# Performance work log

Measured on AMD Instinct MI355X. Metric: run time of the kernel, lower is better.

The kernel has to match this reference:

```python
import jax, jax.numpy as jnp
import numpy as np
import math

MODEL_DIM = 1024
NUM_HEADS = 16
ATTN_DIM = MODEL_DIM // NUM_HEADS  # 64
ROWS, COLS, AXES = 32, 32, 2
PAIRS = ATTN_DIM // (AXES * 2)     # 16
BATCH = 4
TOKENS = ROWS * COLS               # 1024


def setup_inputs() -> dict:
    key = jax.random.key(0)
    ks = jax.random.split(key, 8)
    s = 1.0 / math.sqrt(MODEL_DIM)
    return {
        "x": jax.random.normal(ks[0], (BATCH, TOKENS, MODEL_DIM), jnp.float32),
        "cos": jax.random.uniform(ks[1], (ROWS, COLS, AXES, PAIRS), jnp.float32),
        "sin": jax.random.uniform(ks[2], (ROWS, COLS, AXES, PAIRS), jnp.float32),
        "Wq": jax.random.normal(ks[3], (MODEL_DIM, MODEL_DIM), jnp.float32) * s,
        "Wk": jax.random.normal(ks[4], (MODEL_DIM, MODEL_DIM), jnp.float32) * s,
        "Wv": jax.random.normal(ks[5], (MODEL_DIM, MODEL_DIM), jnp.float32) * s,
        "Wo": jax.random.normal(ks[6], (MODEL_DIM, MODEL_DIM), jnp.float32) * s,
        "bo": jax.random.normal(ks[7], (MODEL_DIM,), jnp.float32) * 0.01,
    }


def _apply_rope(W, cos, sin):
    # W: (b, h, tokens, attn_dim) -> (b, h, rows, cols, axes, pairs, 2)
    b, h, n, d = W.shape
    rows, cols, axes, pairs = cos.shape
    Wp = W.reshape(b, h, rows, cols, axes, pairs, 2)
    c = cos[None, None]
    s = sin[None, None]
    w0, w1 = Wp[..., 0], Wp[..., 1]
    out = jnp.stack([c * w0 - s * w1, s * w0 + c * w1], axis=-1)
    return out.reshape(b, h, n, d)


def reference(x, cos, sin, Wq, Wk, Wv, Wo, bo):
    b, n, _ = x.shape
    # torch Linear: y = x @ W.T
    Q = (x @ Wq.T).reshape(b, n, NUM_HEADS, ATTN_DIM).transpose(0, 2, 1, 3)
    K = (x @ Wk.T).reshape(b, n, NUM_HEADS, ATTN_DIM).transpose(0, 2, 1, 3)
    V = (x @ Wv.T).reshape(b, n, NUM_HEADS, ATTN_DIM).transpose(0, 2, 1, 3)
    Q = _apply_rope(Q, cos, sin)
    K = _apply_rope(K, cos, sin)
    scores = jnp.einsum("bhqd,bhkd->bhqk", Q, K) / math.sqrt(ATTN_DIM)
    attn = jax.nn.softmax(scores, axis=-1)
    o = jnp.einsum("bhqk,bhkd->bhqd", attn, V)
    o = o.transpose(0, 2, 1, 3).reshape(b, n, MODEL_DIM)
    return o @ Wo.T + bo
```

## Files before the change

### kernel.cpp

```cpp
#include <hip/hip_runtime.h>
#include <hip/hip_bf16.h>

typedef __bf16 bf16;
typedef __bf16 bf16x4 __attribute__((ext_vector_type(4)));
typedef __bf16 bf16x8 __attribute__((ext_vector_type(8)));
typedef float  f32x4  __attribute__((ext_vector_type(4)));
typedef unsigned int u32x2 __attribute__((ext_vector_type(2)));

#define MFMA16(a, b, c) __builtin_amdgcn_mfma_f32_16x16x32_bf16((a), (b), (c), 0, 0, 0)

#define GLOBAL_AS(p) ((const __attribute__((address_space(1))) void*)(p))
#define LDS_AS(p)    ((__attribute__((address_space(3))) void*)(p))

#define BATCH 4
#define TOK   1024
#define DIM   1024
#define HEADS 16
#define HD    64
#define MTOT  (BATCH * TOK)
#define MELEM (1024u * 1024u)

__global__ __launch_bounds__(256) void k_prep(
    const float* __restrict__ X,
    const float* __restrict__ W0, const float* __restrict__ W1,
    const float* __restrict__ W2, const float* __restrict__ W3,
    bf16* __restrict__ xh, bf16* __restrict__ wsp)
{
    const int bid = blockIdx.x;
    if (bid < 2048) {
        size_t i0 = ((size_t)bid * 256 + threadIdx.x) * 8;
        f32x4 a = *(const f32x4*)(X + i0);
        f32x4 b = *(const f32x4*)(X + i0 + 4);
        bf16x8 h;
        #pragma unroll
        for (int j = 0; j < 4; j++) { h[j] = (bf16)a[j]; h[4 + j] = (bf16)b[j]; }
        *(bf16x8*)(xh + i0) = h;
    } else {
        const int b2 = bid - 2048;
        const int widx = b2 >> 9;
        const int inner = b2 & 511;
        const float* W = (widx == 0) ? W0 : (widx == 1) ? W1 : (widx == 2) ? W2 : W3;
        size_t i0 = ((size_t)inner * 256 + threadIdx.x) * 8;
        f32x4 a = *(const f32x4*)(W + i0);
        f32x4 b = *(const f32x4*)(W + i0 + 4);
        bf16x8 h, l;
        #pragma unroll
        for (int j = 0; j < 4; j++) {
            bf16 g0 = (bf16)a[j]; h[j] = g0;     l[j] = (bf16)(a[j] - (float)g0);
            bf16 g1 = (bf16)b[j]; h[4 + j] = g1; l[4 + j] = (bf16)(b[j] - (float)g1);
        }
        *(bf16x8*)(wsp + (size_t)widx * MELEM + i0) = h;
        if (widx == 3)
            *(bf16x8*)(wsp + 4 * (size_t)MELEM + i0) = l;
    }
}

__global__ __launch_bounds__(512) void k_gemmQKV(
    const bf16* __restrict__ Ag, const bf16* __restrict__ wsp,
    const float* __restrict__ cosT, const float* __restrict__ sinT,
    bf16* __restrict__ q_o, bf16* __restrict__ k_o, bf16* __restrict__ v_o)
{
    __shared__ bf16 Alin[128 * 64];
    __shared__ bf16 Blin[256 * 64];

    const int fid = blockIdx.x;
    const int swz = (fid & 7) * 48 + (fid >> 3);
    const int nt = swz % 12;
    const int mt = swz / 12;

    const int t = threadIdx.x;
    const int lane = t & 63;
    const int w = t >> 6;
    const int wr = w >> 2, wc = w & 3;
    const int l15 = lane & 15;

    f32x4 acc[4][4];
    #pragma unroll
    for (int m = 0; m < 4; m++)
        #pragma unroll
        for (int n = 0; n < 4; n++)
            #pragma unroll
            for (int r = 0; r < 4; r++) acc[m][n][r] = 0.f;

    const int srow = lane >> 3;
    const int schk8 = ((lane & 7) ^ (srow & 7)) * 8;
    const bf16* asrc = Ag  + (size_t)(mt * 128 + srow) * DIM + schk8;
    const bf16* bsrc = wsp + (size_t)(nt * 256 + srow) * DIM + schk8;

    for (int k0 = 0; k0 < DIM; k0 += 64) {
        __syncthreads();
        #pragma unroll
        for (int ii = 0; ii < 2; ++ii) {
            int i = w * 2 + ii;
            __builtin_amdgcn_global_load_lds(
                GLOBAL_AS(asrc + (size_t)i * 8 * DIM + k0),
                LDS_AS(&Alin[i * 512]), 16, 0, 0);
        }
        #pragma unroll
        for (int jj = 0; jj < 4; ++jj) {
            int j = w * 4 + jj;
            __builtin_amdgcn_global_load_lds(
                GLOBAL_AS(bsrc + (size_t)j * 8 * DIM + k0),
                LDS_AS(&Blin[j * 512]), 16, 0, 0);
        }
        __syncthreads();

        #pragma unroll
        for (int ks = 0; ks < 2; ks++) {
            const int cc = (lane >> 4) + ks * 4;
            bf16x8 fb[4];
            #pragma unroll
            for (int n = 0; n < 4; n++) {
                int rb = wc * 64 + n * 16 + l15;
                fb[n] = *(const bf16x8*)&Blin[rb * 64 + ((cc ^ (rb & 7)) << 3)];
            }
            #pragma unroll
            for (int m = 0; m < 4; m++) {
                int r = wr * 64 + m * 16 + l15;
                bf16x8 fa = *(const bf16x8*)&Alin[r * 64 + ((cc ^ (r & 7)) << 3)];
                #pragma unroll
                for (int n = 0; n < 4; n++)
                    acc[m][n] = MFMA16(fa, fb[n], acc[m][n]);
            }
        }
    }

    const int mode = nt >> 2;
    const int h = (nt & 3) * 4 + wc;
    if (mode == 2) {
        #pragma unroll
        for (int m = 0; m < 4; m++) {
            const int grow0 = mt * 128 + wr * 64 + m * 16 + (lane >> 4) * 4;
            const int b = grow0 >> 10, ntok0 = grow0 & (TOK - 1);
            #pragma unroll
            for (int n = 0; n < 4; n++) {
                const int d = n * 16 + l15;
                bf16x4 pk;
                #pragma unroll
                for (int r = 0; r < 4; r++) pk[r] = (bf16)acc[m][n][r];
                *(bf16x4*)&v_o[((size_t)((b * HEADS + h) * HD + d)) * TOK + ntok0] = pk;
            }
        }
    } else {
        __syncthreads();
        float* cosL = (float*)Alin;
        float* sinL = (float*)Blin;
        const int tb = (mt & 7) * 128;
        *(f32x4*)(cosL + t * 8)     = *(const f32x4*)(cosT + (size_t)tb * 32 + t * 8);
        *(f32x4*)(cosL + t * 8 + 4) = *(const f32x4*)(cosT + (size_t)tb * 32 + t * 8 + 4);
        *(f32x4*)(sinL + t * 8)     = *(const f32x4*)(sinT + (size_t)tb * 32 + t * 8);
        *(f32x4*)(sinL + t * 8 + 4) = *(const f32x4*)(sinT + (size_t)tb * 32 + t * 8 + 4);
        __syncthreads();

        bf16* dst = (mode == 0) ? q_o : k_o;
        const float sc = (mode == 0) ? 0.18033688f : 1.0f;
        #pragma unroll
        for (int m = 0; m < 4; m++) {
            const int grow0 = mt * 128 + wr * 64 + m * 16 + (lane >> 4) * 4;
            const int b = grow0 >> 10, ntok0 = grow0 & (TOK - 1);
            const int loc0 = wr * 64 + m * 16 + (lane >> 4) * 4;
            #pragma unroll
            for (int n = 0; n < 4; n++) {
                const int d = n * 16 + l15;
                const int idp = (d >> 5) * 16 + ((d >> 1) & 15);
                const bool ev = (d & 1) == 0;
                #pragma unroll
                for (int r = 0; r < 4; r++) {
                    float v = acc[m][n][r];
                    float pr = __shfl_xor(v, 1, 64);
                    float c = cosL[(loc0 + r) * 32 + idp];
                    float s = sinL[(loc0 + r) * 32 + idp];
                    float res = (ev ? (c * v - s * pr) : (s * pr + c * v)) * sc;
                    dst[((size_t)(b * HEADS + h) * TOK + ntok0 + r) * HD + d] = (bf16)res;
                }
            }
        }
    }
}

__global__ __launch_bounds__(256) void k_gemmO(
    const bf16* __restrict__ Ag, const bf16* __restrict__ wsp,
    const float* __restrict__ bo, float* __restrict__ f_o)
{
    __shared__ bf16 Alin[64 * 64];
    __shared__ bf16 Bhlin[128 * 64];
    __shared__ bf16 Bllin[128 * 64];

    const bf16* Bh_g = wsp + 3 * (size_t)MELEM;
    const bf16* Bl_g = wsp + 4 * (size_t)MELEM;

    const int fid = blockIdx.x;
    const int swz = (fid & 7) * 64 + (fid >> 3);
    const int nt = swz & 7;
    const int mt = swz >> 3;

    const int t = threadIdx.x;
    const int lane = t & 63;
    const int w = t >> 6;
    const int wr = w >> 1, wc = w & 1;
    const int l15 = lane & 15;

    f32x4 acc[2][4];
    #pragma unroll
    for (int m = 0; m < 2; m++)
        #pragma unroll
        for (int n = 0; n < 4; n++)
            #pragma unroll
            for (int r = 0; r < 4; r++) acc[m][n][r] = 0.f;

    const int srow = lane >> 3;
    const int schk8 = ((lane & 7) ^ (srow & 7)) * 8;
    const bf16* asrc  = Ag   + (size_t)(mt * 64 + srow) * DIM + schk8;
    const bf16* bhsrc = Bh_g + (size_t)(nt * 128 + srow) * DIM + schk8;
    const bf16* blsrc = Bl_g + (size_t)(nt * 128 + srow) * DIM + schk8;

    for (int k0 = 0; k0 < DIM; k0 += 64) {
        __syncthreads();
        #pragma unroll
        for (int ii = 0; ii < 2; ++ii) {
            int i = w * 2 + ii;
            __builtin_amdgcn_global_load_lds(
                GLOBAL_AS(asrc + (size_t)i * 8 * DIM + k0),
                LDS_AS(&Alin[i * 512]), 16, 0, 0);
        }
        #pragma unroll
        for (int jj = 0; jj < 4; ++jj) {
            int j = w * 4 + jj;
            size_t roff = (size_t)j * 8 * DIM + k0;
            __builtin_amdgcn_global_load_lds(GLOBAL_AS(bhsrc + roff),
                                             LDS_AS(&Bhlin[j * 512]), 16, 0, 0);
            __builtin_amdgcn_global_load_lds(GLOBAL_AS(blsrc + roff),
                                             LDS_AS(&Bllin[j * 512]), 16, 0, 0);
        }
        __syncthreads();

        #pragma unroll
        for (int ks = 0; ks < 2; ks++) {
            const int cc = (lane >> 4) + ks * 4;
            bf16x8 fbh[4], fbl[4];
            #pragma unroll
            for (int n = 0; n < 4; n++) {
                int r = wc * 64 + n * 16 + l15;
                int off = r * 64 + ((cc ^ (r & 7)) << 3);
                fbh[n] = *(const bf16x8*)&Bhlin[off];
                fbl[n] = *(const bf16x8*)&Bllin[off];
            }
            #pragma unroll
            for (int m = 0; m < 2; m++) {
                int r = wr * 32 + m * 16 + l15;
                bf16x8 fa = *(const bf16x8*)&Alin[r * 64 + ((cc ^ (r & 7)) << 3)];
                #pragma unroll
                for (int n = 0; n < 4; n++) {
                    acc[m][n] = MFMA16(fa, fbh[n], acc[m][n]);
                    acc[m][n] = MFMA16(fa, fbl[n], acc[m][n]);
                }
            }
        }
    }

    #pragma unroll
    for (int m = 0; m < 2; m++) {
        #pragma unroll
        for (int n = 0; n < 4; n++) {
            const int grow0 = mt * 64 + wr * 32 + m * 16 + (lane >> 4) * 4;
            const int gcol  = nt * 128 + wc * 64 + n * 16 + l15;
            const float bias = bo[gcol];
            #pragma unroll
            for (int r = 0; r < 4; r++)
                f_o[(size_t)(grow0 + r) * DIM + gcol] = acc[m][n][r] + bias;
        }
    }
}

__global__ __launch_bounds__(256) void k_attn(
    const bf16* __restrict__ Q, const bf16* __restrict__ K,
    const bf16* __restrict__ Vt, bf16* __restrict__ O)
{
    __shared__ bf16 Ks0[64 * 64];
    __shared__ bf16 Ks1[64 * 64];
    __shared__ bf16 Vs0[64 * 64];
    __shared__ bf16 Vs1[64 * 64];
    __shared__ bf16 Ps[64 * 64];

    const int fid = blockIdx.x;
    const int swz = (fid & 7) * 128 + (fid >> 3);
    const int qt = swz & 15;
    const int bh = swz >> 4;

    const int t = threadIdx.x;
    const int lane = t & 63;
    const int w = t >> 6;
    const int col = lane & 15;
    const int grp = lane >> 4;
    const int m7 = col & 7;
    const int qrow = w * 16 + col;

    const bf16* qp = Q + ((size_t)bh * TOK + qt * 64 + qrow) * HD + grp * 8;
    bf16x8 qf0 = *(const bf16x8*)qp;
    bf16x8 qf1 = *(const bf16x8*)(qp + 32);

    const int srow = lane >> 3;
    const int schk8 = ((lane & 7) ^ (srow & 7)) * 8;
    const bf16* ksrc = K  + ((size_t)bh * TOK + srow) * HD + schk8;
    const bf16* vsrc = Vt + ((size_t)bh * HD + srow) * TOK + schk8;

    bf16x8 ones;
    #pragma unroll
    for (int j = 0; j < 8; j++) ones[j] = (bf16)1.0f;

    f32x4 zero = {0.f, 0.f, 0.f, 0.f};
    f32x4 lacc = zero;
    f32x4 o_[4];
    #pragma unroll
    for (int dt = 0; dt < 4; dt++) o_[dt] = zero;

    unsigned int* PsU = (unsigned int*)Ps;

    auto stage = [&](int kt, bf16* kb, bf16* vb) {
        #pragma unroll
        for (int ii = 0; ii < 2; ++ii) {
            int i = w * 2 + ii;
            __builtin_amdgcn_global_load_lds(
                GLOBAL_AS(ksrc + (size_t)(kt * 64 + i * 8) * HD),
                LDS_AS(kb + i * 512), 16, 0, 0);
            __builtin_amdgcn_global_load_lds(
                GLOBAL_AS(vsrc + (size_t)(i * 8) * TOK + kt * 64),
                LDS_AS(vb + i * 512), 16, 0, 0);
        }
    };

    auto compute = [&](const bf16* kb, const bf16* vb) {
        f32x4 s[4];
        #pragma unroll
        for (int ct = 0; ct < 4; ct++) s[ct] = zero;
        __builtin_amdgcn_s_setprio(1);
        #pragma unroll
        for (int ct = 0; ct < 4; ct++) {
            int rbase = (ct * 16 + col) * 64;
            bf16x8 kf0 = *(const bf16x8*)&kb[rbase + ((grp ^ m7) << 3)];
            bf16x8 kf1 = *(const bf16x8*)&kb[rbase + (((grp + 4) ^ m7) << 3)];
            s[ct] = MFMA16(kf0, qf0, s[ct]);
            s[ct] = MFMA16(kf1, qf1, s[ct]);
        }
        __builtin_amdgcn_s_setprio(0);

        #pragma unroll
        for (int ct = 0; ct < 4; ct++) {
            float p0 = exp2f(s[ct][0]);
            float p1 = exp2f(s[ct][1]);
            float p2 = exp2f(s[ct][2]);
            float p3 = exp2f(s[ct][3]);
            unsigned int a0, a1;
            asm("v_cvt_pk_bf16_f32 %0, %1, %2" : "=v"(a0) : "v"(p0), "v"(p1));
            asm("v_cvt_pk_bf16_f32 %0, %1, %2" : "=v"(a1) : "v"(p2), "v"(p3));
            int cs = (2 * ct + (grp >> 1)) ^ m7;
            u32x2 st = {a0, a1};
            *(u32x2*)&PsU[qrow * 32 + cs * 4 + (grp & 1) * 2] = st;
        }

        __builtin_amdgcn_s_setprio(1);
        #pragma unroll
        for (int tt = 0; tt < 2; tt++) {
            const int coff = ((4 * tt + grp) ^ m7) << 3;
            bf16x8 pf = *(const bf16x8*)&Ps[qrow * 64 + coff];
            lacc = MFMA16(ones, pf, lacc);
            #pragma unroll
            for (int dt = 0; dt < 4; dt++) {
                bf16x8 vf = *(const bf16x8*)&vb[(dt * 16 + col) * 64 + coff];
                o_[dt] = MFMA16(vf, pf, o_[dt]);
            }
        }
        __builtin_amdgcn_s_setprio(0);
    };

    stage(0, Ks0, Vs0);
    #pragma unroll 1
    for (int kk = 0; kk < 8; kk++) {
        __syncthreads();
        stage(2 * kk + 1, Ks1, Vs1);
        compute(Ks0, Vs0);
        __syncthreads();
        if (kk < 7) stage(2 * kk + 2, Ks0, Vs0);
        compute(Ks1, Vs1);
    }

    const float inv = 1.0f / lacc[0];

    const int b = bh >> 4, h = bh & 15;
    const int ntok = qt * 64 + qrow;
    #pragma unroll
    for (int dt = 0; dt < 4; dt++) {
        bf16x4 pk4;
        #pragma unroll
        for (int r = 0; r < 4; r++) pk4[r] = (bf16)(o_[dt][r] * inv);
        *(bf16x4*)&O[((size_t)b * TOK + ntok) * DIM + h * HD + dt * 16 + grp * 4] = pk4;
    }
}

extern "C" void kernel_launch(void* const* d_in, const int* in_sizes, int n_in,
                              void* d_out, int out_size, void* d_ws, size_t ws_size,
                              hipStream_t stream)
{
    const float* x    = (const float*)d_in[0];
    const float* cosT = (const float*)d_in[1];
    const float* sinT = (const float*)d_in[2];
    const float* Wq   = (const float*)d_in[3];
    const float* Wk   = (const float*)d_in[4];
    const float* Wv   = (const float*)d_in[5];
    const float* Wo   = (const float*)d_in[6];
    const float* bo   = (const float*)d_in[7];
    float* out = (float*)d_out;

    bf16* xh  = (bf16*)d_ws;
    bf16* qw  = xh + 4 * (size_t)MELEM;
    bf16* kw  = qw + 4 * (size_t)MELEM;
    bf16* vw  = kw + 4 * (size_t)MELEM;
    bf16* wsp = vw + 4 * (size_t)MELEM;
    bf16* ow  = xh;

    k_prep<<<dim3(4096), dim3(256), 0, stream>>>(x, Wq, Wk, Wv, Wo, xh, wsp);
    k_gemmQKV<<<dim3(384), dim3(512), 0, stream>>>(xh, wsp, cosT, sinT, qw, kw, vw);
    k_attn<<<dim3(1024), dim3(256), 0, stream>>>(qw, kw, vw, ow);
    k_gemmO<<<dim3(512), dim3(256), 0, stream>>>(ow, wsp, bo, out);
}
```

Measured before the change: 98.80 us.

## Double-buffer QKV GEMM LDS tiles with BK=32 and async prefetch

Restructures the QKV projection GEMM main loop into a two-stage double-buffered pipeline. K-tiles drop from 64 to 32 and use a new XOR swizzle, and the global_load_lds for the next tile is issued before computing the current one. s_setprio is added around the MFMA block. The goal is to hide global-to-LDS load latency behind MFMA work. In exchange there are twice as many barriers per K step, and the swizzle must stay correct for the new 32-wide rows.

```diff
diff --git a/kernel.cpp b/kernel.cpp
--- a/kernel.cpp
+++ b/kernel.cpp
@@ -60,8 +60,11 @@
     const float* __restrict__ cosT, const float* __restrict__ sinT,
     bf16* __restrict__ q_o, bf16* __restrict__ k_o, bf16* __restrict__ v_o)
 {
-    __shared__ bf16 Alin[128 * 64];
-    __shared__ bf16 Blin[256 * 64];
+    __shared__ bf16 lds[24576];
+    bf16* A0 = lds;
+    bf16* A1 = lds + 4096;
+    bf16* B0 = lds + 8192;
+    bf16* B1 = lds + 16384;
 
     const int fid = blockIdx.x;
     const int swz = (fid & 7) * 48 + (fid >> 3);
@@ -73,6 +76,7 @@
     const int w = t >> 6;
     const int wr = w >> 2, wc = w & 3;
     const int l15 = lane & 15;
+    const int grp = lane >> 4;
 
     f32x4 acc[4][4];
     #pragma unroll
@@ -82,47 +86,53 @@
             #pragma unroll
             for (int r = 0; r < 4; r++) acc[m][n][r] = 0.f;
 
-    const int srow = lane >> 3;
-    const int schk8 = ((lane & 7) ^ (srow & 7)) * 8;
+    const int srow = lane >> 2;
+    const int schk8 = ((lane & 3) ^ ((lane >> 3) & 3)) * 8;
     const bf16* asrc = Ag  + (size_t)(mt * 128 + srow) * DIM + schk8;
     const bf16* bsrc = wsp + (size_t)(nt * 256 + srow) * DIM + schk8;
 
-    for (int k0 = 0; k0 < DIM; k0 += 64) {
-        __syncthreads();
-        #pragma unroll
-        for (int ii = 0; ii < 2; ++ii) {
-            int i = w * 2 + ii;
+    auto stage = [&](int k, bf16* ab, bf16* bb) {
+        const int k0 = k * 32;
+        __builtin_amdgcn_global_load_lds(
+            GLOBAL_AS(asrc + (size_t)w * 16 * DIM + k0),
+            LDS_AS(ab + w * 512), 16, 0, 0);
+        #pragma unroll
+        for (int jj = 0; jj < 2; ++jj) {
+            int j = w * 2 + jj;
             __builtin_amdgcn_global_load_lds(
-                GLOBAL_AS(asrc + (size_t)i * 8 * DIM + k0),
-                LDS_AS(&Alin[i * 512]), 16, 0, 0);
-        }
-        #pragma unroll
-        for (int jj = 0; jj < 4; ++jj) {
-            int j = w * 4 + jj;
-            __builtin_amdgcn_global_load_lds(
-                GLOBAL_AS(bsrc + (size_t)j * 8 * DIM + k0),
-                LDS_AS(&Blin[j * 512]), 16, 0, 0);
-        }
-        __syncthreads();
-
-        #pragma unroll
-        for (int ks = 0; ks < 2; ks++) {
-            const int cc = (lane >> 4) + ks * 4;
-            bf16x8 fb[4];
-            #pragma unroll
-            for (int n = 0; n < 4; n++) {
-                int rb = wc * 64 + n * 16 + l15;
-                fb[n] = *(const bf16x8*)&Blin[rb * 64 + ((cc ^ (rb & 7)) << 3)];
-            }
-            #pragma unroll
-            for (int m = 0; m < 4; m++) {
-                int r = wr * 64 + m * 16 + l15;
-                bf16x8 fa = *(const bf16x8*)&Alin[r * 64 + ((cc ^ (r & 7)) << 3)];
-                #pragma unroll
-                for (int n = 0; n < 4; n++)
-                    acc[m][n] = MFMA16(fa, fb[n], acc[m][n]);
-            }
-        }
+                GLOBAL_AS(bsrc + (size_t)j * 16 * DIM + k0),
+                LDS_AS(bb + j * 512), 16, 0, 0);
+        }
+    };
+
+    auto compute = [&](const bf16* ab, const bf16* bb) {
+        bf16x8 fb[4];
+        #pragma unroll
+        for (int n = 0; n < 4; n++) {
+            int rb = wc * 64 + n * 16 + l15;
+            fb[n] = *(const bf16x8*)&bb[rb * 32 + ((grp ^ ((rb >> 1) & 3)) << 3)];
+        }
+        __builtin_amdgcn_s_setprio(1);
+        #pragma unroll
+        for (int m = 0; m < 4; m++) {
+            int r = wr * 64 + m * 16 + l15;
+            bf16x8 fa = *(const bf16x8*)&ab[r * 32 + ((grp ^ ((r >> 1) & 3)) << 3)];
+            #pragma unroll
+            for (int n = 0; n < 4; n++)
+                acc[m][n] = MFMA16(fa, fb[n], acc[m][n]);
+        }
+        __builtin_amdgcn_s_setprio(0);
+    };
+
+    stage(0, A0, B0);
+    #pragma unroll 1
+    for (int kk = 0; kk < 16; kk++) {
+        __syncthreads();
+        stage(2 * kk + 1, A1, B1);
+        compute(A0, B0);
+        __syncthreads();
+        if (kk < 15) stage(2 * kk + 2, A0, B0);
+        compute(A1, B1);
     }
 
     const int mode = nt >> 2;
@@ -130,7 +140,7 @@
     if (mode == 2) {
         #pragma unroll
         for (int m = 0; m < 4; m++) {
-            const int grow0 = mt * 128 + wr * 64 + m * 16 + (lane >> 4) * 4;
+            const int grow0 = mt * 128 + wr * 64 + m * 16 + grp * 4;
             const int b = grow0 >> 10, ntok0 = grow0 & (TOK - 1);
             #pragma unroll
             for (int n = 0; n < 4; n++) {
@@ -143,8 +153,8 @@
         }
     } else {
         __syncthreads();
-        float* cosL = (float*)Alin;
-        float* sinL = (float*)Blin;
+        float* cosL = (float*)lds;
+        float* sinL = (float*)(lds + 8192);
         const int tb = (mt & 7) * 128;
         *(f32x4*)(cosL + t * 8)     = *(const f32x4*)(cosT + (size_t)tb * 32 + t * 8);
         *(f32x4*)(cosL + t * 8 + 4) = *(const f32x4*)(cosT + (size_t)tb * 32 + t * 8 + 4);
@@ -156,9 +166,9 @@
         const float sc = (mode == 0) ? 0.18033688f : 1.0f;
         #pragma unroll
         for (int m = 0; m < 4; m++) {
-            const int grow0 = mt * 128 + wr * 64 + m * 16 + (lane >> 4) * 4;
+            const int grow0 = mt * 128 + wr * 64 + m * 16 + grp * 4;
             const int b = grow0 >> 10, ntok0 = grow0 & (TOK - 1);
-            const int loc0 = wr * 64 + m * 16 + (lane >> 4) * 4;
+            const int loc0 = wr * 64 + m * 16 + grp * 4;
             #pragma unroll
             for (int n = 0; n < 4; n++) {
                 const int d = n * 16 + l15;
```

Result: no change. 99.79 us (median of 2 runs) (+1.0%).
